# Kernel optimization log

Hardware: AMD Instinct MI355X
Metric: run time of the kernel (lower is better)

Reference implementation:

```python
import jax, jax.numpy as jnp
import numpy as np

FORGET_BIAS = 1.0


def _lstm_layer(x, lengths, W, b):
    """Single TF-style LSTM layer over time with sequence-length masking.

    x: [B, T, D]; W: [D+H, 4H]; b: [4H]; lengths: [B] int.
    Gate order matches tf.contrib.rnn.LSTMCell: i, j(cell cand), f, o.
    Returns ys [B, T, H], final (h, c) each [B, H].
    """
    B, T, _ = x.shape
    H = W.shape[1] // 4
    h0 = jnp.zeros((B, H), x.dtype)
    c0 = jnp.zeros((B, H), x.dtype)
    lens = lengths.astype(jnp.int32)

    def step(carry, inp):
        h, c = carry
        x_t, t = inp
        z = jnp.concatenate([x_t, h], axis=-1) @ W + b  # [B, 4H]
        i, j, f, o = jnp.split(z, 4, axis=-1)
        new_c = c * jax.nn.sigmoid(f + FORGET_BIAS) + jax.nn.sigmoid(i) * jnp.tanh(j)
        new_h = jnp.tanh(new_c) * jax.nn.sigmoid(o)
        mask = (t < lens)[:, None]  # dynamic_rnn: hold state / zero output past length
        h = jnp.where(mask, new_h, h)
        c = jnp.where(mask, new_c, c)
        out = jnp.where(mask, new_h, jnp.zeros_like(new_h))
        return (h, c), out

    (h_f, c_f), ys = jax.lax.scan(step, (h0, c0), (x.transpose(1, 0, 2), jnp.arange(T)))
    return ys.transpose(1, 0, 2), h_f, c_f


def setup_inputs() -> dict:
    key = jax.random.key(0)
    ks = jax.random.split(key, 5)
    B, T, D, H = 64, 512, 1024, 1024
    x = jax.random.normal(ks[0], (B, T, D), dtype=jnp.float32)
    lengths = jax.random.randint(ks[1], (B,), 1, T + 1).astype(jnp.int64)
    scale = 0.05
    W0 = jax.random.normal(ks[2], (D + H, 4 * H), dtype=jnp.float32) * scale
    b0 = jnp.zeros((4 * H,), dtype=jnp.float32)
    W1 = jax.random.normal(ks[3], (H + H, 4 * H), dtype=jnp.float32) * scale
    b1 = jnp.zeros((4 * H,), dtype=jnp.float32)
    return {"x": x, "lengths": lengths, "W0": W0, "b0": b0, "W1": W1, "b1": b1}


def reference(x, lengths, W0, b0, W1, b1):
    y0, h0, c0 = _lstm_layer(x, lengths, W0, b0)
    y1, h1, c1 = _lstm_layer(y0, lengths, W1, b1)
    h_stack = jnp.stack([h0, h1])  # [nlayers, B, H]
    c_stack = jnp.stack([c0, c1])
    return y1, h_stack, c_stack
```

## Files before the change

kernel.cpp:

```cpp
#include <hip/hip_runtime.h>
#include <stdint.h>

#define NWG   128
#define NTHR  512
#define Tsz   512

typedef __attribute__((ext_vector_type(8))) short short8;
typedef __attribute__((ext_vector_type(4))) float f32x4;
typedef __attribute__((ext_vector_type(4))) unsigned uintx4;

__device__ __forceinline__ unsigned short f2bf(float f) {
    unsigned u = __builtin_bit_cast(unsigned, f);
    u += 0x7fffu + ((u >> 16) & 1u);
    return (unsigned short)(u >> 16);
}
__device__ __forceinline__ float sigm(float x) {
    float e = __expf(-__builtin_fabsf(x));
    float r = 1.0f / (1.0f + e);
    return x >= 0.0f ? r : 1.0f - r;
}
__device__ __forceinline__ float tanh_(float x) {
    float e = __expf(-2.0f * __builtin_fabsf(x));
    float r = (1.0f - e) / (1.0f + e);
    return x >= 0.0f ? r : -r;
}

__device__ __forceinline__ void st16_cc(unsigned short* p, uintx4 v) {
    asm volatile("global_store_dwordx4 %0, %1, off sc0 sc1" :: "v"(p), "v"(v) : "memory");
}
__device__ __forceinline__ void st4_cc(unsigned* p, unsigned v) {
    asm volatile("global_store_dword %0, %1, off sc0 sc1" :: "v"(p), "v"(v) : "memory");
}
__device__ __forceinline__ void drain_vm() {
    asm volatile("s_waitcnt vmcnt(0)" ::: "memory");
}
__device__ __forceinline__ unsigned ld4_cc(const unsigned* p) {
    unsigned v;
    asm volatile("global_load_dword %0, %1, off sc0 sc1\n\t"
                 "s_waitcnt vmcnt(0)"
                 : "=&v"(v) : "v"(p) : "memory");
    return v;
}

__global__ void cast_x(const float* __restrict__ x, unsigned short* __restrict__ xb) {
    int o = blockIdx.x * 256 + threadIdx.x;
    int t = o >> 13;
    int r = o & 8191;
    int kb = r >> 6;
    int b  = r & 63;
    const float* s = x + (((size_t)b * Tsz + t) * 1024 + kb * 8);
    float4 f0 = ((const float4*)s)[0];
    float4 f1 = ((const float4*)s)[1];
    unsigned short tmp[8];
    tmp[0] = f2bf(f0.x); tmp[1] = f2bf(f0.y); tmp[2] = f2bf(f0.z); tmp[3] = f2bf(f0.w);
    tmp[4] = f2bf(f1.x); tmp[5] = f2bf(f1.y); tmp[6] = f2bf(f1.z); tmp[7] = f2bf(f1.w);
    ((uint4*)xb)[o] = *(const uint4*)tmp;
}

__global__ void build_wc(const float* __restrict__ W0, const float* __restrict__ W1,
                         unsigned short* __restrict__ wc0, unsigned short* __restrict__ wc1) {
    int o = blockIdx.x * 256 + threadIdx.x;
    int layer = o >> 20;
    int r = o & 1048575;
    int w  = r >> 13;
    int r2 = r & 8191;
    int kb = r2 >> 5;
    int n  = r2 & 31;
    int nt = n >> 4, n16 = n & 15;
    int g = n16 >> 2, q = n16 & 3;
    int col = g * 1024 + w * 8 + nt * 4 + q;
    const float* W = layer ? W1 : W0;
    unsigned short* wc = layer ? wc1 : wc0;
    unsigned short tmp[8];
#pragma unroll
    for (int i = 0; i < 8; ++i) tmp[i] = f2bf(W[(size_t)(kb * 8 + i) * 4096 + col]);
    ((uint4*)wc)[r] = *(const uint4*)tmp;
}

__global__ void build_pb(const float* __restrict__ b0, const float* __restrict__ b1,
                         float* __restrict__ pb, unsigned* __restrict__ flg) {
    int o = blockIdx.x * 256 + threadIdx.x;
    if (o < 2048) flg[o] = 0u;
    int layer = o >> 12;
    int r = o & 4095;
    int w = r >> 5;
    int n = r & 31;
    int nt = n >> 4, n16 = n & 15;
    int g = n16 >> 2, q = n16 & 3;
    const float* bb = layer ? b1 : b0;
    pb[o] = bb[g * 1024 + w * 8 + nt * 4 + q];
}

__device__ __forceinline__ void gbar(unsigned* flg, unsigned& bseq, int w, int tid) {
    ++bseq;
    __syncthreads();
    if (tid == 0) st4_cc(flg + w * 16, bseq);
    if (tid < 128) {
        while (ld4_cc(flg + tid * 16) < bseq) __builtin_amdgcn_s_sleep(1);
    }
    __syncthreads();
}
__device__ __forceinline__ void gbar_full(unsigned* flg, unsigned& bseq, int w, int tid) {
    ++bseq;
    __syncthreads();
    if (tid == 0) { __threadfence(); st4_cc(flg + w * 16, bseq); }
    if (tid < 128) {
        while (ld4_cc(flg + tid * 16) < bseq) __builtin_amdgcn_s_sleep(1);
    }
    __syncthreads();
    if (tid == 0) __threadfence();
    __syncthreads();
}

__device__ __forceinline__ void gemm512(const unsigned short* a0p,
                                        const short8* lb,
                                        f32x4& c00, f32x4& c01, f32x4& c10, f32x4& c11) {
    short8 A0[16], A1[16];
#pragma unroll
    for (int s = 0; s < 16; ++s) {
        A0[s] = *(const short8*)(a0p + s * 2048);
        A1[s] = *(const short8*)(a0p + s * 2048 + 128);
    }
#pragma unroll
    for (int s = 0; s < 16; ++s) {
        short8 bf0 = lb[s * 128];
        short8 bf1 = lb[s * 128 + 16];
        c00 = __builtin_amdgcn_mfma_f32_16x16x32_bf16(A0[s], bf0, c00, 0, 0, 0);
        c01 = __builtin_amdgcn_mfma_f32_16x16x32_bf16(A0[s], bf1, c01, 0, 0, 0);
        c10 = __builtin_amdgcn_mfma_f32_16x16x32_bf16(A1[s], bf0, c10, 0, 0, 0);
        c11 = __builtin_amdgcn_mfma_f32_16x16x32_bf16(A1[s], bf1, c11, 0, 0, 0);
    }
}

__launch_bounds__(NTHR, 2)
__global__ void lstm_loop(const unsigned short* __restrict__ xb,
                          unsigned short* __restrict__ y0b,
                          const unsigned short* __restrict__ wc0,
                          const unsigned short* __restrict__ wc1,
                          const float* __restrict__ pb,
                          const int* __restrict__ lens,
                          unsigned short* __restrict__ hring,
                          float* __restrict__ cst,
                          unsigned* __restrict__ flg,
                          float* __restrict__ out) {
    extern __shared__ short8 lwc[];
    __shared__ float zbuf[3][64][33];
    __shared__ float pbl[2][32];
    __shared__ __align__(16) unsigned short hsh[64][8];

    const int w = blockIdx.x;
    const int tid = threadIdx.x;
    const int lane = tid & 63;
    const int wave = tid >> 6;
    const int m     = wave & 1;
    const int khalf = (wave >> 1) & 1;
    const int op    = wave >> 2;
    const int q16 = lane >> 4;
    const int n16 = lane & 15;

    const int aoff = ((khalf * 64 + q16) * 64 + m * 32 + n16) * 8;
    const short8* lb = lwc + ((op * 128 + khalf * 64 + q16) * 32 + n16);

    if (tid < 256) {
        st4_cc((unsigned*)hring + w * 256 + tid, 0u);
        int ly = tid >> 7, r = tid & 127;
        ((float4*)(cst + ly * 65536 + w * 512))[r] = make_float4(0.f, 0.f, 0.f, 0.f);
    }
    if (tid < 64) pbl[tid >> 5][tid & 31] = pb[((tid >> 5) * 128 + w) * 32 + (tid & 31)];
    const int lenb = lens[tid & 63];
    drain_vm();
    unsigned bseq = 0;
    gbar_full(flg, bseq, w, tid);

    for (int layer = 0; layer < 2; ++layer) {
        const unsigned short* xsrc = layer ? y0b : xb;
        const unsigned short* wc   = layer ? wc1 : wc0;

        {
            const short8* gsrc = (const short8*)(wc + (size_t)w * 65536);
#pragma unroll 4
            for (int i = 0; i < 16; ++i) lwc[tid + i * 512] = gsrc[tid + i * 512];
        }
        __syncthreads();

        float hpf = 0.f;
        const int b  = tid & 63;
        const int jj = wave;
        const int cb = (jj >> 2) * 16 + (jj & 3);

        for (int t = 0; t < Tsz; ++t) {
            f32x4 c00 = {0.f,0.f,0.f,0.f}, c01 = {0.f,0.f,0.f,0.f};
            f32x4 c10 = {0.f,0.f,0.f,0.f}, c11 = {0.f,0.f,0.f,0.f};
            const unsigned short* Abase = op ? (hring + (size_t)t * 65536)
                                             : (xsrc  + (size_t)t * 65536);
            gemm512(Abase + aoff, lb, c00, c01, c10, c11);

            const int rowb = m * 32 + q16 * 4;
            if (!(op == 0 && khalf == 1)) {
                const int slice = op ? (1 + khalf) : 0;
#pragma unroll
                for (int r = 0; r < 4; ++r) {
                    zbuf[slice][rowb + r][n16]           = c00[r];
                    zbuf[slice][rowb + r][n16 + 16]      = c01[r];
                    zbuf[slice][rowb + 16 + r][n16]      = c10[r];
                    zbuf[slice][rowb + 16 + r][n16 + 16] = c11[r];
                }
            }
            __syncthreads();
            if (op == 0 && khalf == 1) {
#pragma unroll
                for (int r = 0; r < 4; ++r) {
                    zbuf[0][rowb + r][n16]           += c00[r];
                    zbuf[0][rowb + r][n16 + 16]      += c01[r];
                    zbuf[0][rowb + 16 + r][n16]      += c10[r];
                    zbuf[0][rowb + 16 + r][n16 + 16] += c11[r];
                }
            }
            __syncthreads();

            const bool active = (t < lenb);
            {
                float zi = zbuf[0][b][cb]      + zbuf[1][b][cb]      + zbuf[2][b][cb]      + pbl[layer][cb];
                float zc = zbuf[0][b][cb + 4]  + zbuf[1][b][cb + 4]  + zbuf[2][b][cb + 4]  + pbl[layer][cb + 4];
                float zf = zbuf[0][b][cb + 8]  + zbuf[1][b][cb + 8]  + zbuf[2][b][cb + 8]  + pbl[layer][cb + 8];
                float zo = zbuf[0][b][cb + 12] + zbuf[1][b][cb + 12] + zbuf[2][b][cb + 12] + pbl[layer][cb + 12];
                if (active) {
                    const int ci = (layer * 1024 + w * 8 + jj) * 64 + b;
                    float cc = cst[ci];
                    float cn = cc * sigm(zf + 1.0f) + sigm(zi) * tanh_(zc);
                    cst[ci] = cn;
                    hpf = tanh_(cn) * sigm(zo);
                }
                unsigned short hv = f2bf(hpf);
                hsh[b][jj] = hv;
                const int hi = (w * 64 + b) * 8 + jj;
                if (layer == 0) {
                    y0b[(size_t)t * 65536 + hi] = active ? hv : (unsigned short)0;
                } else {
                    out[(size_t)(b * Tsz + t) * 1024 + w * 8 + jj] = active ? hpf : 0.0f;
                }
            }
            __syncthreads();
            if (tid < 64) {
                uintx4 v = ((const uintx4*)hsh)[tid];
                st16_cc((unsigned short*)hring + (size_t)(t + 1) * 65536
                        + (size_t)w * 512 + (size_t)tid * 8, v);
                drain_vm();
            }
            gbar(flg, bseq, w, tid);
        }
        {
            const int j = w * 8 + jj;
            out[33554432 + layer * 65536 + b * 1024 + j]          = hpf;
            out[33554432 + 131072 + layer * 65536 + b * 1024 + j] = cst[(layer * 1024 + j) * 64 + b];
        }
        if (layer == 0) {
            if (tid < 256) st4_cc((unsigned*)hring + w * 256 + tid, 0u);
            drain_vm();
            gbar_full(flg, bseq, w, tid);
        }
    }
}

extern "C" void kernel_launch(void* const* d_in, const int* in_sizes, int n_in,
                              void* d_out, int out_size, void* d_ws, size_t ws_size,
                              hipStream_t stream) {
    const float* x    = (const float*)d_in[0];
    const int*   lens = (const int*)d_in[1];
    const float* W0   = (const float*)d_in[2];
    const float* b0   = (const float*)d_in[3];
    const float* W1   = (const float*)d_in[4];
    const float* b1   = (const float*)d_in[5];
    char* ws = (char*)d_ws;

    unsigned short* xb   = (unsigned short*)(ws);
    unsigned short* y0b  = (unsigned short*)(ws + 67108864);
    unsigned short* wc0  = (unsigned short*)(ws + 134217728);
    unsigned short* wc1  = (unsigned short*)(ws + 150994944);
    float*          pb   = (float*)         (ws + 167772160);
    float*          cst  = (float*)         (ws + 167804928);
    unsigned*       flg  = (unsigned*)      (ws + 168329216);
    unsigned short* hrng = (unsigned short*)(ws + 168337408);

    hipLaunchKernelGGL(cast_x,   dim3(16384), dim3(256), 0, stream, x, xb);
    hipLaunchKernelGGL(build_wc, dim3(8192),  dim3(256), 0, stream, W0, W1, wc0, wc1);
    hipLaunchKernelGGL(build_pb, dim3(32),    dim3(256), 0, stream, b0, b1, pb, flg);

    float* out = (float*)d_out;
    void* args[] = { &xb, &y0b, &wc0, &wc1, &pb, &lens, &hrng, &cst, &flg, &out };
    (void)hipLaunchCooperativeKernel((void*)lstm_loop, dim3(NWG), dim3(NTHR), args,
                                     131072 , stream);
}
```

Before: 7.670 ms.

## Prefetch next-step x tiles, keep cell state in registers, trim barriers

Input-projection waves now load the next timestep's x tile from global memory before the barrier, so that load overlaps the rest of the step while the recurrent waves still fetch h each step. The cell state lives in a per-thread register instead of a global cst array, which removes a global read and write per step. __syncthreads is replaced with an lgkmcnt wait plus s_barrier, and the global barrier is folded inline and moved to waves 4-5. The prefetch raises register pressure under 2-block launch bounds, and the lighter barrier relies on the vmcnt drains being in the right places.

```diff
diff --git a/kernel.cpp b/kernel.cpp
--- a/kernel.cpp
+++ b/kernel.cpp
@@ -40,6 +40,9 @@
                  "s_waitcnt vmcnt(0)"
                  : "=&v"(v) : "v"(p) : "memory");
     return v;
+}
+__device__ __forceinline__ void bar_lds() {
+    asm volatile("s_waitcnt lgkmcnt(0)\n\ts_barrier" ::: "memory");
 }
 
 __global__ void cast_x(const float* __restrict__ x, unsigned short* __restrict__ xb) {
@@ -91,15 +94,6 @@
     pb[o] = bb[g * 1024 + w * 8 + nt * 4 + q];
 }
 
-__device__ __forceinline__ void gbar(unsigned* flg, unsigned& bseq, int w, int tid) {
-    ++bseq;
-    __syncthreads();
-    if (tid == 0) st4_cc(flg + w * 16, bseq);
-    if (tid < 128) {
-        while (ld4_cc(flg + tid * 16) < bseq) __builtin_amdgcn_s_sleep(1);
-    }
-    __syncthreads();
-}
 __device__ __forceinline__ void gbar_full(unsigned* flg, unsigned& bseq, int w, int tid) {
     ++bseq;
     __syncthreads();
@@ -112,15 +106,15 @@
     __syncthreads();
 }
 
-__device__ __forceinline__ void gemm512(const unsigned short* a0p,
-                                        const short8* lb,
-                                        f32x4& c00, f32x4& c01, f32x4& c10, f32x4& c11) {
-    short8 A0[16], A1[16];
+__device__ __forceinline__ void issue_a(const unsigned short* a0p, short8 A0[16], short8 A1[16]) {
 #pragma unroll
     for (int s = 0; s < 16; ++s) {
         A0[s] = *(const short8*)(a0p + s * 2048);
         A1[s] = *(const short8*)(a0p + s * 2048 + 128);
     }
+}
+__device__ __forceinline__ void mfma16(const short8 A0[16], const short8 A1[16], const short8* lb,
+                                       f32x4& c00, f32x4& c01, f32x4& c10, f32x4& c11) {
 #pragma unroll
     for (int s = 0; s < 16; ++s) {
         short8 bf0 = lb[s * 128];
@@ -140,7 +134,6 @@
                           const float* __restrict__ pb,
                           const int* __restrict__ lens,
                           unsigned short* __restrict__ hring,
-                          float* __restrict__ cst,
                           unsigned* __restrict__ flg,
                           float* __restrict__ out) {
     extern __shared__ short8 lwc[];
@@ -161,11 +154,7 @@
     const int aoff = ((khalf * 64 + q16) * 64 + m * 32 + n16) * 8;
     const short8* lb = lwc + ((op * 128 + khalf * 64 + q16) * 32 + n16);
 
-    if (tid < 256) {
-        st4_cc((unsigned*)hring + w * 256 + tid, 0u);
-        int ly = tid >> 7, r = tid & 127;
-        ((float4*)(cst + ly * 65536 + w * 512))[r] = make_float4(0.f, 0.f, 0.f, 0.f);
-    }
+    if (tid < 256) st4_cc((unsigned*)hring + w * 256 + tid, 0u);
     if (tid < 64) pbl[tid >> 5][tid & 31] = pb[((tid >> 5) * 128 + w) * 32 + (tid & 31)];
     const int lenb = lens[tid & 63];
     drain_vm();
@@ -184,16 +173,22 @@
         __syncthreads();
 
         float hpf = 0.f;
+        float cpf = 0.f;
         const int b  = tid & 63;
         const int jj = wave;
         const int cb = (jj >> 2) * 16 + (jj & 3);
 
+        short8 A0[16], A1[16];
+        if (op == 0) issue_a(xsrc + aoff, A0, A1);
+
         for (int t = 0; t < Tsz; ++t) {
+            if (op == 1) {
+                issue_a(hring + (size_t)t * 65536 + aoff, A0, A1);
+                __builtin_amdgcn_sched_barrier(0);
+            }
             f32x4 c00 = {0.f,0.f,0.f,0.f}, c01 = {0.f,0.f,0.f,0.f};
             f32x4 c10 = {0.f,0.f,0.f,0.f}, c11 = {0.f,0.f,0.f,0.f};
-            const unsigned short* Abase = op ? (hring + (size_t)t * 65536)
-                                             : (xsrc  + (size_t)t * 65536);
-            gemm512(Abase + aoff, lb, c00, c01, c10, c11);
+            mfma16(A0, A1, lb, c00, c01, c10, c11);
 
             const int rowb = m * 32 + q16 * 4;
             if (!(op == 0 && khalf == 1)) {
@@ -206,7 +201,8 @@
                     zbuf[slice][rowb + 16 + r][n16 + 16] = c11[r];
                 }
             }
-            __syncthreads();
+            if (op == 0 && t + 1 < Tsz) issue_a(xsrc + (size_t)(t + 1) * 65536 + aoff, A0, A1);
+            bar_lds();
             if (op == 0 && khalf == 1) {
 #pragma unroll
                 for (int r = 0; r < 4; ++r) {
@@ -216,7 +212,7 @@
                     zbuf[0][rowb + 16 + r][n16 + 16] += c11[r];
                 }
             }
-            __syncthreads();
+            bar_lds();
 
             const bool active = (t < lenb);
             {
@@ -225,11 +221,8 @@
                 float zf = zbuf[0][b][cb + 8]  + zbuf[1][b][cb + 8]  + zbuf[2][b][cb + 8]  + pbl[layer][cb + 8];
                 float zo = zbuf[0][b][cb + 12] + zbuf[1][b][cb + 12] + zbuf[2][b][cb + 12] + pbl[layer][cb + 12];
                 if (active) {
-                    const int ci = (layer * 1024 + w * 8 + jj) * 64 + b;
-                    float cc = cst[ci];
-                    float cn = cc * sigm(zf + 1.0f) + sigm(zi) * tanh_(zc);
-                    cst[ci] = cn;
-                    hpf = tanh_(cn) * sigm(zo);
+                    cpf = cpf * sigm(zf + 1.0f) + sigm(zi) * tanh_(zc);
+                    hpf = tanh_(cpf) * sigm(zo);
                 }
                 unsigned short hv = f2bf(hpf);
                 hsh[b][jj] = hv;
@@ -240,19 +233,24 @@
                     out[(size_t)(b * Tsz + t) * 1024 + w * 8 + jj] = active ? hpf : 0.0f;
                 }
             }
-            __syncthreads();
-            if (tid < 64) {
-                uintx4 v = ((const uintx4*)hsh)[tid];
+            bar_lds();
+            ++bseq;
+            if (wave == 4) {
+                uintx4 v = ((const uintx4*)hsh)[lane];
                 st16_cc((unsigned short*)hring + (size_t)(t + 1) * 65536
-                        + (size_t)w * 512 + (size_t)tid * 8, v);
+                        + (size_t)w * 512 + (size_t)lane * 8, v);
                 drain_vm();
             }
-            gbar(flg, bseq, w, tid);
+            if (tid == 256) st4_cc(flg + w * 16, bseq);
+            if (tid >= 256 && tid < 384) {
+                while (ld4_cc(flg + (tid - 256) * 16) < bseq) __builtin_amdgcn_s_sleep(1);
+            }
+            bar_lds();
         }
         {
             const int j = w * 8 + jj;
             out[33554432 + layer * 65536 + b * 1024 + j]          = hpf;
-            out[33554432 + 131072 + layer * 65536 + b * 1024 + j] = cst[(layer * 1024 + j) * 64 + b];
+            out[33554432 + 131072 + layer * 65536 + b * 1024 + j] = cpf;
         }
         if (layer == 0) {
             if (tid < 256) st4_cc((unsigned*)hring + w * 256 + tid, 0u);
@@ -278,7 +276,6 @@
     unsigned short* wc0  = (unsigned short*)(ws + 134217728);
     unsigned short* wc1  = (unsigned short*)(ws + 150994944);
     float*          pb   = (float*)         (ws + 167772160);
-    float*          cst  = (float*)         (ws + 167804928);
     unsigned*       flg  = (unsigned*)      (ws + 168329216);
     unsigned short* hrng = (unsigned short*)(ws + 168337408);
 
@@ -287,7 +284,7 @@
     hipLaunchKernelGGL(build_pb, dim3(32),    dim3(256), 0, stream, b0, b1, pb, flg);
 
     float* out = (float*)d_out;
-    void* args[] = { &xb, &y0b, &wc0, &wc1, &pb, &lens, &hrng, &cst, &flg, &out };
+    void* args[] = { &xb, &y0b, &wc0, &wc1, &pb, &lens, &hrng, &flg, &out };
     (void)hipLaunchCooperativeKernel((void*)lstm_loop, dim3(NWG), dim3(NTHR), args,
                                      131072 , stream);
 }
```

Measured after the change: 6.380 ms. 16.8% less time.
